# Optimization experiments

Measured on AMD Instinct MI355X. Metric: run time of the kernel, lower is better.

## Reference

```python
import jax, jax.numpy as jnp
import numpy as np

N, D, C, K, M = 32768, 512, 64, 16, 128
DEPTH = 4            # log2(K): decision-tree depth per codebook
NODES = K - 1        # 15 internal tree nodes per codebook


def _build_selection_matrix():
    # Node i of the binary tree lives at level log2(i+1) and thresholds the
    # level-l selected dimension of its codebook.
    S = np.zeros((C * NODES, C * DEPTH), dtype=np.float32)
    base = np.zeros((NODES, DEPTH), dtype=np.float32)
    for i in range(NODES):
        base[i, int(np.log2(i + 1))] = 1.0
    for c in range(C):
        S[c * NODES:(c + 1) * NODES, c * DEPTH:(c + 1) * DEPTH] = base
    return S


def _build_bit_matrix():
    # Leaf k scores +1/-1 on each of its DEPTH ancestor nodes; the true leaf
    # attains the maximal score DEPTH.
    base = np.zeros((K, NODES), dtype=np.float32)
    for k in range(K):
        for l in range(DEPTH):
            node = (1 << l) - 1 + (k >> (DEPTH - l))   # ancestor at level l
            bit = (k >> (DEPTH - 1 - l)) & 1            # right(1)/left(0)
            base[k, node] = 1.0 if bit else -1.0
    B = np.zeros((C * K, C * NODES), dtype=np.float32)
    for c in range(C):
        B[c * K:(c + 1) * K, c * NODES:(c + 1) * NODES] = base
    return B


def setup_inputs() -> dict:
    key = jax.random.key(0)
    k1, k2, k3, k4 = jax.random.split(key, 4)
    I = jax.random.normal(k1, (N, D), jnp.float32)
    T = jax.random.normal(k2, (C * NODES,), jnp.float32) * 0.1   # thresholds
    L = jax.random.normal(k3, (M, C, K), jnp.float32)            # LUT
    dims = jnp.sort(jax.random.randint(k4, (C * DEPTH,), 0, D))  # selected cols
    S = jnp.asarray(_build_selection_matrix())
    B = jnp.asarray(_build_bit_matrix())
    temp = jnp.ones((1,), jnp.float32)
    return {"I": I, "T": T, "L": L, "S": S, "B": B, "dims": dims, "temp": temp}


def reference(I, T, L, S, B, dims, temp):
    t = temp[0]
    x_sel = I[:, dims]                                  # (N, C*DEPTH) gather
    h = x_sel @ S.T - T                                 # (N, C*NODES)
    tanh_h = jnp.tanh(h / t)
    # straight-through sign: forward sign(h), backward d(tanh(h/t))
    sign_ste = jnp.sign(h) - jax.lax.stop_gradient(tanh_h) + tanh_h
    b = sign_ste @ B.T                                  # (N, C*K) leaf scores
    soft = jax.nn.softmax(b.reshape(-1, C, K) / t, axis=2)
    hard = jax.nn.one_hot(jnp.argmax(soft, axis=2), K, dtype=soft.dtype)
    # straight-through one-hot encoding E: forward hard, backward soft
    E = hard - jax.lax.stop_gradient(soft) + soft       # (N, C, K)
    return jnp.einsum("nck,mck->nm", E, L)              # LUT gather-sum readout
```

## Files before the change

### kernel.cpp

```cpp
#include <hip/hip_runtime.h>

#define N_TOTAL 32768
#define D_DIM   512
#define C_DIM   64
#define M_DIM   128
#define NODES_  15
#define ROWS_B  128
#define NSUB    8

typedef unsigned short u16;
typedef unsigned int   u32;
typedef unsigned long long u64;
typedef unsigned char  u8;
typedef float  f32x4   __attribute__((ext_vector_type(4)));
typedef short  short8v __attribute__((ext_vector_type(8)));

#define WAIT_VM(N) asm volatile("s_waitcnt vmcnt(" #N ")" ::: "memory")

__device__ __forceinline__ u32 f2bf_bits(float f) {
    u32 u = __float_as_uint(f);
    return (u + 0x7FFFu + ((u >> 16) & 1u)) >> 16;
}

__device__ __forceinline__ void lds_barrier() {
    asm volatile("s_waitcnt lgkmcnt(0)" ::: "memory");
    __builtin_amdgcn_s_barrier();
    asm volatile("" ::: "memory");
}

__device__ __forceinline__ void gload_lds16(const float* g, float* l) {
    __builtin_amdgcn_global_load_lds(
        (const __attribute__((address_space(1))) void*)g,
        (__attribute__((address_space(3))) void*)l, 16, 0, 0);
}

__global__ __launch_bounds__(256) void build_lbf(
    const float* __restrict__ L, u16* __restrict__ Lbf)
{
    int idx  = blockIdx.x * 256 + threadIdx.x;
    int lane = idx & 63;
    int ch   = (idx >> 6) & 31;
    int ct   = idx >> 11;
    int m  = ct * 16 + (lane & 15);
    int k0 = ch * 32 + ((lane >> 4) * 8);
    const float* src = L + (size_t)m * 1024 + k0;
    float4 a = *(const float4*)(src);
    float4 b = *(const float4*)(src + 4);
    u32 w0 = f2bf_bits(a.x) | (f2bf_bits(a.y) << 16);
    u32 w1 = f2bf_bits(a.z) | (f2bf_bits(a.w) << 16);
    u32 w2 = f2bf_bits(b.x) | (f2bf_bits(b.y) << 16);
    u32 w3 = f2bf_bits(b.z) | (f2bf_bits(b.w) << 16);
    *(uint4*)(Lbf + (size_t)idx * 8) = make_uint4(w0, w1, w2, w3);
}

__global__ __launch_bounds__(512, 2) void mega_kernel(
    const float* __restrict__ I,
    const float* __restrict__ T,
    const int* __restrict__ dims,
    const u16* __restrict__ Lbf,
    float* __restrict__ out)
{
    __shared__ float sI[2][16 * D_DIM];
    __shared__ float sT[C_DIM * NODES_];
    __shared__ u8    sC[2][C_DIM * 20];

    const int tid  = threadIdx.x;
    const int lane = tid & 63;
    const int wv   = tid >> 6;
    const int rowBase = blockIdx.x * ROWS_B;

    const int4 dml = ((const int4*)dims)[lane];

    uint4 Breg[32];
    #pragma unroll
    for (int ch = 0; ch < 32; ++ch)
        Breg[ch] = *(const uint4*)(Lbf + ((size_t)(wv * 32 + ch) * 64 + lane) * 8);

    auto issue = [&](int t) {
        const float* src = I + (size_t)(rowBase + t * 16 + wv * 2) * D_DIM;
        float* dst = &sI[t & 1][wv * 2 * D_DIM];
        #pragma unroll
        for (int i = 0; i < 4; ++i)
            gload_lds16(src + i * 256 + lane * 4, dst + i * 256);
    };

    const float* tc = sT + lane * NODES_;

    auto descend_write = [&](int t) {
        u32 pk = 0;
        #pragma unroll
        for (int rr = 0; rr < 2; ++rr) {
            const float* v = &sI[t & 1][(wv * 2 + rr) * D_DIM];
            float x0 = v[dml.x], x1 = v[dml.y], x2 = v[dml.z], x3 = v[dml.w];
            int node = 0, k = 0;
            int b0 = (x0 - tc[0] > 0.0f) ? 1 : 0;
            k = b0; node = 1 + b0;
            int b1 = (x1 - tc[node] > 0.0f) ? 1 : 0;
            k = (k << 1) | b1; node = (node << 1) + 1 + b1;
            int b2 = (x2 - tc[node] > 0.0f) ? 1 : 0;
            k = (k << 1) | b2; node = (node << 1) + 1 + b2;
            int b3 = (x3 - tc[node] > 0.0f) ? 1 : 0;
            k = (k << 1) | b3;
            pk |= (u32)k << (8 * rr);
        }
        *(u16*)(&sC[t & 1][lane * 20 + wv * 2]) = (u16)pk;
    };

    const int l15     = lane & 15;
    const int clsLane = (lane >> 5) & 1;
    const int kb      = ((lane >> 4) & 1) * 8;

    auto gemm_store = [&](int t) {
        f32x4 acc = {0.f, 0.f, 0.f, 0.f};
        const u8* cb = &sC[t & 1][0];
        #pragma unroll
        for (int ch = 0; ch < 32; ++ch) {
            const int cls = ch * 2 + clsLane;
            u32 cd = cb[cls * 20 + l15];
            u32 tt = cd - (u32)kb;
            u64 sv = 0x3F80ull << ((tt & 3) * 16);
            union { u64 d[2]; short8v v; } a;
            a.d[0] = (tt < 4) ? sv : 0ull;
            a.d[1] = (tt >= 4 && tt < 8) ? sv : 0ull;
            union { uint4 u; short8v v; } b;
            b.u = Breg[ch];
            acc = __builtin_amdgcn_mfma_f32_16x16x32_bf16(a.v, b.v, acc, 0, 0, 0);
        }
        int r0 = rowBase + t * 16 + ((lane >> 4) << 2);
        float* o = out + (size_t)r0 * M_DIM + wv * 16 + l15;
        o[0 * M_DIM] = acc[0];
        o[1 * M_DIM] = acc[1];
        o[2 * M_DIM] = acc[2];
        o[3 * M_DIM] = acc[3];
    };

    issue(0); issue(1);
    for (int j = tid; j < C_DIM * NODES_; j += 512) sT[j] = T[j];
    __syncthreads();
    descend_write(0);
    lds_barrier();

    for (int t = 0; t < NSUB - 1; ++t) {
        gemm_store(t);
        if (t < NSUB - 2) {
            issue(t + 2);
            WAIT_VM(4);
        } else {
            WAIT_VM(0);
        }
        descend_write(t + 1);
        lds_barrier();
    }
    gemm_store(NSUB - 1);
}

extern "C" void kernel_launch(void* const* d_in, const int* in_sizes, int n_in,
                              void* d_out, int out_size, void* d_ws, size_t ws_size,
                              hipStream_t stream) {
    const float* I    = (const float*)d_in[0];
    const float* T    = (const float*)d_in[1];
    const float* L    = (const float*)d_in[2];
    const int*   dims = (const int*)d_in[5];

    u16* Lbf = (u16*)d_ws;

    hipLaunchKernelGGL(build_lbf, dim3(64), dim3(256), 0, stream, L, Lbf);
    hipLaunchKernelGGL(mega_kernel, dim3(N_TOTAL / ROWS_B), dim3(512), 0, stream,
                       I, T, dims, Lbf, (float*)d_out);
}
```

Before: 128.9 us.

## Split tree descent and LUT GEMM into phases, streaming LUT per chunk

The kernel now does all eight tree-descent sub-tiles first, keeping the I-row loads double-buffered, and stores every code in a single enlarged code buffer. Only then does it run the MFMA readout, looping over codebook chunks with eight row-tile accumulators. The LUT fragment is loaded from global memory once per chunk instead of held as 32 preloaded registers. This cuts the per-sub-tile barriers and the large register footprint, but it gives up overlap between descent and GEMM and adds global LUT loads in the inner loop.

```diff
diff --git a/kernel.cpp b/kernel.cpp
--- a/kernel.cpp
+++ b/kernel.cpp
@@ -6,7 +6,7 @@
 #define M_DIM   128
 #define NODES_  15
 #define ROWS_B  128
-#define NSUB    8
+#define NCHUNK  8
 
 typedef unsigned short u16;
 typedef unsigned int   u32;
@@ -20,12 +20,6 @@
 __device__ __forceinline__ u32 f2bf_bits(float f) {
     u32 u = __float_as_uint(f);
     return (u + 0x7FFFu + ((u >> 16) & 1u)) >> 16;
-}
-
-__device__ __forceinline__ void lds_barrier() {
-    asm volatile("s_waitcnt lgkmcnt(0)" ::: "memory");
-    __builtin_amdgcn_s_barrier();
-    asm volatile("" ::: "memory");
 }
 
 __device__ __forceinline__ void gload_lds16(const float* g, float* l) {
@@ -62,7 +56,7 @@
 {
     __shared__ float sI[2][16 * D_DIM];
     __shared__ float sT[C_DIM * NODES_];
-    __shared__ u8    sC[2][C_DIM * 20];
+    __shared__ u8    sC[C_DIM * 132];
 
     const int tid  = threadIdx.x;
     const int lane = tid & 63;
@@ -70,11 +64,6 @@
     const int rowBase = blockIdx.x * ROWS_B;
 
     const int4 dml = ((const int4*)dims)[lane];
-
-    uint4 Breg[32];
-    #pragma unroll
-    for (int ch = 0; ch < 32; ++ch)
-        Breg[ch] = *(const uint4*)(Lbf + ((size_t)(wv * 32 + ch) * 64 + lane) * 8);
 
     auto issue = [&](int t) {
         const float* src = I + (size_t)(rowBase + t * 16 + wv * 2) * D_DIM;
@@ -103,55 +92,57 @@
             k = (k << 1) | b3;
             pk |= (u32)k << (8 * rr);
         }
-        *(u16*)(&sC[t & 1][lane * 20 + wv * 2]) = (u16)pk;
+        *(u16*)(sC + lane * 132 + t * 16 + wv * 2) = (u16)pk;
     };
+
+    issue(0); issue(1);
+    for (int j = tid; j < C_DIM * NODES_; j += 512) sT[j] = T[j];
+    __syncthreads();
+    descend_write(0); issue(2);
+    descend_write(1); issue(3);
+    WAIT_VM(4); descend_write(2); issue(4);
+    WAIT_VM(4); descend_write(3); issue(5);
+    WAIT_VM(4); descend_write(4); issue(6);
+    WAIT_VM(4); descend_write(5); issue(7);
+    WAIT_VM(4); descend_write(6);
+    WAIT_VM(0); descend_write(7);
+    __syncthreads();
 
     const int l15     = lane & 15;
     const int clsLane = (lane >> 5) & 1;
     const int kb      = ((lane >> 4) & 1) * 8;
 
-    auto gemm_store = [&](int t) {
-        f32x4 acc = {0.f, 0.f, 0.f, 0.f};
-        const u8* cb = &sC[t & 1][0];
+    f32x4 acc[8] = {};
+    const u16* lbW = Lbf + ((size_t)wv * 32 * 64 + lane) * 8;
+
+    #pragma unroll 4
+    for (int ch = 0; ch < 32; ++ch) {
+        union { uint4 u; short8v v; } b;
+        b.u = *(const uint4*)(lbW + (size_t)ch * 64 * 8);
+        const int cls = ch * 2 + clsLane;
+        const u8* cb = sC + cls * 132;
         #pragma unroll
-        for (int ch = 0; ch < 32; ++ch) {
-            const int cls = ch * 2 + clsLane;
-            u32 cd = cb[cls * 20 + l15];
+        for (int rt = 0; rt < 8; ++rt) {
+            u32 cd = cb[rt * 16 + l15];
             u32 tt = cd - (u32)kb;
             u64 sv = 0x3F80ull << ((tt & 3) * 16);
             union { u64 d[2]; short8v v; } a;
             a.d[0] = (tt < 4) ? sv : 0ull;
             a.d[1] = (tt >= 4 && tt < 8) ? sv : 0ull;
-            union { uint4 u; short8v v; } b;
-            b.u = Breg[ch];
-            acc = __builtin_amdgcn_mfma_f32_16x16x32_bf16(a.v, b.v, acc, 0, 0, 0);
+            acc[rt] = __builtin_amdgcn_mfma_f32_16x16x32_bf16(
+                          a.v, b.v, acc[rt], 0, 0, 0);
         }
-        int r0 = rowBase + t * 16 + ((lane >> 4) << 2);
+    }
+
+    #pragma unroll
+    for (int rt = 0; rt < 8; ++rt) {
+        int r0 = rowBase + rt * 16 + ((lane >> 4) << 2);
         float* o = out + (size_t)r0 * M_DIM + wv * 16 + l15;
-        o[0 * M_DIM] = acc[0];
-        o[1 * M_DIM] = acc[1];
-        o[2 * M_DIM] = acc[2];
-        o[3 * M_DIM] = acc[3];
-    };
-
-    issue(0); issue(1);
-    for (int j = tid; j < C_DIM * NODES_; j += 512) sT[j] = T[j];
-    __syncthreads();
-    descend_write(0);
-    lds_barrier();
-
-    for (int t = 0; t < NSUB - 1; ++t) {
-        gemm_store(t);
-        if (t < NSUB - 2) {
-            issue(t + 2);
-            WAIT_VM(4);
-        } else {
-            WAIT_VM(0);
-        }
-        descend_write(t + 1);
-        lds_barrier();
+        o[0 * M_DIM] = acc[rt][0];
+        o[1 * M_DIM] = acc[rt][1];
+        o[2 * M_DIM] = acc[rt][2];
+        o[3 * M_DIM] = acc[rt][3];
     }
-    gemm_store(NSUB - 1);
 }
 
 extern "C" void kernel_launch(void* const* d_in, const int* in_sizes, int n_in,
```

Result: no change. 126.7 us (-1.7%).
